# Optimization experiments

Measured on AMD Instinct MI355X. Metric: run time of the kernel, lower is better.

The kernel has to match this reference:

```python
import jax, jax.numpy as jnp
import numpy as np

NUM_MODELS = 64
IN_F, HID, OUT_F = 6, 64, 3
LAYERS = 5
LN_EPS = 1e-5


def _mm_linear(x, W, B, idx):
    # W: [M, out, in], B: [M, out], x: [N, in], idx: [N]
    return jnp.einsum('nof,nf->no', W[idx], x) + B[idx]


def _mm_layernorm(x, g, b, idx):
    mu = jnp.mean(x, axis=-1, keepdims=True)
    var = jnp.mean((x - mu) ** 2, axis=-1, keepdims=True)
    xn = (x - mu) * jax.lax.rsqrt(var + LN_EPS)
    return xn * g[idx] + b[idx]


def setup_inputs() -> dict:
    key = jax.random.key(0)
    ks = jax.random.split(key, 16)
    N = 262144
    sqrt_k = float(np.sqrt(1.0 / NUM_MODELS))
    u = lambda k, shape: jax.random.uniform(k, shape, jnp.float32, -sqrt_k, sqrt_k)
    inp = {
        'x': jax.random.normal(ks[0], (N, IN_F), jnp.float32),
        'indices': jax.random.randint(ks[1], (N,), 0, NUM_MODELS),
        'W0': u(ks[2], (NUM_MODELS, HID, IN_F)), 'B0': u(ks[3], (NUM_MODELS, HID)),
        'G0': jnp.ones((NUM_MODELS, HID), jnp.float32), 'H0': jnp.zeros((NUM_MODELS, HID), jnp.float32),
        'W1': u(ks[4], (NUM_MODELS, HID, HID)), 'B1': u(ks[5], (NUM_MODELS, HID)),
        'G1': jnp.ones((NUM_MODELS, HID), jnp.float32), 'H1': jnp.zeros((NUM_MODELS, HID), jnp.float32),
        'W2': u(ks[6], (NUM_MODELS, HID, HID)), 'B2': u(ks[7], (NUM_MODELS, HID)),
        'G2': jnp.ones((NUM_MODELS, HID), jnp.float32), 'H2': jnp.zeros((NUM_MODELS, HID), jnp.float32),
        'W3': u(ks[8], (NUM_MODELS, HID, HID)), 'B3': u(ks[9], (NUM_MODELS, HID)),
        'G3': jnp.ones((NUM_MODELS, HID), jnp.float32), 'H3': jnp.zeros((NUM_MODELS, HID), jnp.float32),
        'W4': u(ks[10], (NUM_MODELS, OUT_F, HID)), 'B4': u(ks[11], (NUM_MODELS, OUT_F)),
    }
    return inp


def reference(x, indices, W0, B0, G0, H0, W1, B1, G1, H1, W2, B2, G2, H2, W3, B3, G3, H3, W4, B4):
    # forward_through_layers with use_layernorm=True, layers=5:
    Ws = [(W0, B0, G0, H0), (W1, B1, G1, H1), (W2, B2, G2, H2), (W3, B3, G3, H3)]
    h = x
    for W, B, G, Hb in Ws:
        h = _mm_linear(h, W, B, indices)
        h = _mm_layernorm(h, G, Hb, indices)
        h = jax.nn.relu(h)
    return _mm_linear(h, W4, B4, indices)  # [N, 3]
```

## Files before the change

kernel.cpp:

```cpp
#include <hip/hip_runtime.h>


#define NM    64
#define HIDD  64
#define INF   6
#define OUTF  3
#define CAP   4864
#define NBLKB 128

#define CSTRIDE   32
#define O_CURSORS 0
#define O_ORDER   2048
#define IWS_INTS  (O_ORDER + NM * CAP)

#define CONST_B   30720
#define NCONSTF   784
#define IMG_BYTES 33856

#define HST 72

typedef _Float16 v8h __attribute__((ext_vector_type(8)));
typedef _Float16 v4h __attribute__((ext_vector_type(4)));
typedef float    v4f __attribute__((ext_vector_type(4)));

__global__ __launch_bounds__(256, 4) void bucket_img_kernel(
    const int* __restrict__ idx, const float* __restrict__ x, int n,
    const float* __restrict__ W0, const float* __restrict__ W1,
    const float* __restrict__ W2, const float* __restrict__ W3,
    const float* __restrict__ W4,
    const float* __restrict__ B0, const float* __restrict__ G0, const float* __restrict__ H0,
    const float* __restrict__ B1, const float* __restrict__ G1, const float* __restrict__ H1,
    const float* __restrict__ B2, const float* __restrict__ G2, const float* __restrict__ H2,
    const float* __restrict__ B3, const float* __restrict__ G3, const float* __restrict__ H3,
    const float* __restrict__ B4,
    int* __restrict__ iws, _Float16* __restrict__ xs,
    unsigned char* __restrict__ imgbase) {
    __shared__ int lcnt[NM], lcur[NM];
    const int b = blockIdx.x, t = threadIdx.x;
    const int m = b >> 1, sub = b & 1;

    _Float16* img = (_Float16*)(imgbase + (size_t)m * IMG_BYTES);
    float* cst = (float*)(imgbase + (size_t)m * IMG_BYTES + CONST_B);
    for (int s = sub * 256 + t; s < 1920; s += 512) {
        int f = s >> 6, l = s & 63;
        int c = l & 15, q = l >> 4;
        float vals[8];
        if (f < 4) {
            const float* wr = W0 + m * 384 + (f * 16 + c) * 6;
#pragma unroll
            for (int j = 0; j < 8; j++) {
                int k = q * 8 + j;
                vals[j] = (k < INF) ? wr[k] : 0.0f;
            }
        } else if (f < 28) {
            int ll = (f - 4) >> 3, fb = (f - 4) & 7;
            int mt = fb >> 1, kh = fb & 1;
            const float* W = (ll == 0) ? W1 : (ll == 1) ? W2 : W3;
            const float* wr = W + m * 4096 + (mt * 16 + c) * 64 + kh * 32 + q * 8;
#pragma unroll
            for (int j = 0; j < 8; j++) vals[j] = wr[j];
        } else {
            int kh = f - 28;
            const float* wr = W4 + m * 192 + c * 64 + kh * 32 + q * 8;
#pragma unroll
            for (int j = 0; j < 8; j++) vals[j] = (c < OUTF) ? wr[j] : 0.0f;
        }
        v8h o;
#pragma unroll
        for (int j = 0; j < 8; j++) o[j] = (_Float16)vals[j];
        *(v8h*)(img + (size_t)s * 8) = o;
    }
    for (int e = sub * 256 + t; e < NCONSTF; e += 512) {
        const float* lsrc[12] = {B0, G0, H0, B1, G1, H1, B2, G2, H2, B3, G3, H3};
        float v = 0.0f;
        if (e < 768) {
            int l = e / 192, r = e - l * 192;
            v = lsrc[l * 3 + (r >> 6)][m * 64 + (r & 63)];
        } else if (e < 771) {
            v = B4[m * 3 + (e - 768)];
        }
        cst[e] = v;
    }

    if (t < NM) lcnt[t] = 0;
    __syncthreads();
    const int per = (n + NBLKB - 1) / NBLKB;
    const int beg = b * per, end = min(n, beg + per);
    for (int i = beg + t; i < end; i += 256) atomicAdd(&lcnt[idx[i]], 1);
    __syncthreads();
    if (t < NM) lcur[t] = atomicAdd(&iws[O_CURSORS + t * CSTRIDE], lcnt[t]);
    __syncthreads();
    for (int i = beg + t; i < end; i += 256) {
        int mm = idx[i];
        int r = atomicAdd(&lcur[mm], 1);
        int slot = mm * CAP + r;
        iws[O_ORDER + slot] = i;
        const float* xp = x + (size_t)i * 6;
        float2 a0 = *(const float2*)(xp);
        float2 a1 = *(const float2*)(xp + 2);
        float2 a2 = *(const float2*)(xp + 4);
        v8h o = {};
        o[0] = (_Float16)a0.x; o[1] = (_Float16)a0.y;
        o[2] = (_Float16)a1.x; o[3] = (_Float16)a1.y;
        o[4] = (_Float16)a2.x; o[5] = (_Float16)a2.y;
        *(v8h*)(xs + (size_t)slot * 8) = o;
    }
}

__device__ __forceinline__ void layer_epilogue(v4f D[4], const v4f gg[4], const v4f hh[4],
                                               _Float16* __restrict__ st) {
    float S = 0.0f, Q2 = 0.0f;
#pragma unroll
    for (int mt = 0; mt < 4; mt++)
#pragma unroll
        for (int r = 0; r < 4; r++) {
            float v = D[mt][r];
            S += v;
            Q2 = fmaf(v, v, Q2);
        }
    S += __shfl_xor(S, 16, 64);
    S += __shfl_xor(S, 32, 64);
    Q2 += __shfl_xor(Q2, 16, 64);
    Q2 += __shfl_xor(Q2, 32, 64);
    float mu = S * (1.0f / 64.0f);
    float var = Q2 * (1.0f / 64.0f) - mu * mu;
    float rs = rsqrtf(var + 1e-5f);
#pragma unroll
    for (int mt = 0; mt < 4; mt++) {
        v4h o;
#pragma unroll
        for (int r = 0; r < 4; r++) {
            float a = gg[mt][r] * rs;
            float bb = fmaf(-mu, a, hh[mt][r]);
            o[r] = (_Float16)fmaxf(fmaf(D[mt][r], a, bb), 0.0f);
        }
        *(v4h*)(st + mt * 16) = o;
    }
}

__global__ __launch_bounds__(256, 4) void mlp_kernel(
    const int* __restrict__ iws, const _Float16* __restrict__ xs,
    const unsigned char* __restrict__ imgbase, float* __restrict__ out) {
    __shared__ __align__(16) _Float16 s_H[4 * 64 * HST];

    const int m = blockIdx.y;
    const int cnt = iws[O_CURSORS + m * CSTRIDE];
    const int beg = m * CAP, end = beg + cnt;
    const int base = beg + blockIdx.x * 256;
    if (base >= end) return;

    const int t = threadIdx.x, w = t >> 6, lane = t & 63;
    const int c = lane & 15, q = lane >> 4;
    const int wbase = base + w * 64;
    if (wbase >= end) return;

    const _Float16* img = (const _Float16*)(imgbase + (size_t)m * IMG_BYTES);
    const float* cf = (const float*)(imgbase + (size_t)m * IMG_BYTES + CONST_B);
    _Float16* Hw = s_H + w * (64 * HST);
    const int* order = iws + O_ORDER;

    int sid[4], sp[4];
#pragma unroll
    for (int ti = 0; ti < 4; ti++) {
        int p = wbase + ti * 16 + c;
        sp[ti] = p < end ? p : end - 1;
        sid[ti] = order[sp[ti]];
    }

    {
        v8h A[4];
#pragma unroll
        for (int mt = 0; mt < 4; mt++)
            A[mt] = *(const v8h*)(img + mt * 512 + lane * 8);
        v4f bias[4], gg[4], hh[4];
#pragma unroll
        for (int mt = 0; mt < 4; mt++) {
            bias[mt] = *(const v4f*)(cf + mt * 16 + q * 4);
            gg[mt]   = *(const v4f*)(cf + 64 + mt * 16 + q * 4);
            hh[mt]   = *(const v4f*)(cf + 128 + mt * 16 + q * 4);
        }
#pragma unroll
        for (int ti = 0; ti < 4; ti++) {
            v8h bfr = {};
            if (q == 0) bfr = *(const v8h*)(xs + (size_t)sp[ti] * 8);
            v4f D[4];
#pragma unroll
            for (int mt = 0; mt < 4; mt++)
                D[mt] = __builtin_amdgcn_mfma_f32_16x16x32_f16(A[mt], bfr, bias[mt], 0, 0, 0);
            layer_epilogue(D, gg, hh, Hw + (ti * 16 + c) * HST + q * 4);
        }
    }

#pragma unroll
    for (int l = 1; l <= 3; l++) {
        const _Float16* wp = img + 2048 + (l - 1) * 4096 + lane * 8;
        v8h A[4][2];
#pragma unroll
        for (int mt = 0; mt < 4; mt++)
#pragma unroll
            for (int kh = 0; kh < 2; kh++)
                A[mt][kh] = *(const v8h*)(wp + (mt * 2 + kh) * 512);
        const float* cb = cf + l * 192;
        v4f bias[4], gg[4], hh[4];
#pragma unroll
        for (int mt = 0; mt < 4; mt++) {
            bias[mt] = *(const v4f*)(cb + mt * 16 + q * 4);
            gg[mt]   = *(const v4f*)(cb + 64 + mt * 16 + q * 4);
            hh[mt]   = *(const v4f*)(cb + 128 + mt * 16 + q * 4);
        }
#pragma unroll
        for (int ti = 0; ti < 4; ti++) {
            const _Float16* hp = Hw + (ti * 16 + c) * HST;
            v8h b0 = *(const v8h*)(hp + q * 8);
            v8h b1 = *(const v8h*)(hp + 32 + q * 8);
            v4f D[4];
#pragma unroll
            for (int mt = 0; mt < 4; mt++) {
                D[mt] = __builtin_amdgcn_mfma_f32_16x16x32_f16(A[mt][0], b0, bias[mt], 0, 0, 0);
                D[mt] = __builtin_amdgcn_mfma_f32_16x16x32_f16(A[mt][1], b1, D[mt], 0, 0, 0);
            }
            layer_epilogue(D, gg, hh, Hw + (ti * 16 + c) * HST + q * 4);
        }
    }

    {
        const _Float16* wp = img + 14336 + lane * 8;
        v8h A0 = *(const v8h*)(wp);
        v8h A1 = *(const v8h*)(wp + 512);
        v4f b4i = {cf[768], cf[769], cf[770], 0.0f};
#pragma unroll
        for (int ti = 0; ti < 4; ti++) {
            const _Float16* hp = Hw + (ti * 16 + c) * HST;
            v8h b0 = *(const v8h*)(hp + q * 8);
            v8h b1 = *(const v8h*)(hp + 32 + q * 8);
            v4f D = __builtin_amdgcn_mfma_f32_16x16x32_f16(A0, b0, b4i, 0, 0, 0);
            D = __builtin_amdgcn_mfma_f32_16x16x32_f16(A1, b1, D, 0, 0, 0);
            int p = wbase + ti * 16 + c;
            if (q == 0 && p < end) {
                float* op = out + (size_t)sid[ti] * 3;
                op[0] = D[0]; op[1] = D[1]; op[2] = D[2];
            }
        }
    }
}

extern "C" void kernel_launch(void* const* d_in, const int* in_sizes, int n_in,
                              void* d_out, int out_size, void* d_ws, size_t ws_size,
                              hipStream_t stream) {
    const float* x  = (const float*)d_in[0];
    const int*  idx = (const int*)d_in[1];
    const float* W0 = (const float*)d_in[2];
    const float* B0 = (const float*)d_in[3];
    const float* G0 = (const float*)d_in[4];
    const float* H0 = (const float*)d_in[5];
    const float* W1 = (const float*)d_in[6];
    const float* B1 = (const float*)d_in[7];
    const float* G1 = (const float*)d_in[8];
    const float* H1 = (const float*)d_in[9];
    const float* W2 = (const float*)d_in[10];
    const float* B2 = (const float*)d_in[11];
    const float* G2 = (const float*)d_in[12];
    const float* H2 = (const float*)d_in[13];
    const float* W3 = (const float*)d_in[14];
    const float* B3 = (const float*)d_in[15];
    const float* G3 = (const float*)d_in[16];
    const float* H3 = (const float*)d_in[17];
    const float* W4 = (const float*)d_in[18];
    const float* B4 = (const float*)d_in[19];
    float* out = (float*)d_out;

    int n = in_sizes[1];
    int* iws = (int*)d_ws;
    _Float16* xs = (_Float16*)((char*)d_ws + (size_t)IWS_INTS * 4);
    unsigned char* imgbase =
        (unsigned char*)d_ws + (size_t)IWS_INTS * 4 + (size_t)NM * CAP * 16;

    hipMemsetAsync(d_ws, 0, NM * CSTRIDE * sizeof(int), stream);
    bucket_img_kernel<<<dim3(NBLKB), 256, 0, stream>>>(
        idx, x, n, W0, W1, W2, W3, W4,
        B0, G0, H0, B1, G1, H1, B2, G2, H2, B3, G3, H3, B4, iws, xs, imgbase);
    mlp_kernel<<<dim3(19, NM), 256, 0, stream>>>(iws, xs, imgbase, out);
}
```

Baseline: 136.5 us.

## Split bucket cursors four ways and halve MLP tile per wave

The bucketing kernel now uses 256 blocks, each assigned to one of four cursor classes per model. Each class fills its own region of the bucket, two growing from each end of a half, which spreads atomic contention on the global cursors. Local ranks are computed in a single pass and kept in registers, removing the second idx read and the shared-memory atomics. The MLP kernel processes 32 rows per wave instead of 64 over a doubled grid, loads LayerNorm gamma and beta inside the epilogue to cut register use, and raises the launch bound to 6 blocks per SIMD for more occupancy. Rows in gaps between the regions are skipped by validity masks, at the cost of more complex bounds logic and possibly idle waves.

Result: slower. 176.4 us (+29.2%).

```diff
diff --git a/kernel.cpp b/kernel.cpp
--- a/kernel.cpp
+++ b/kernel.cpp
@@ -6,11 +6,12 @@
 #define INF   6
 #define OUTF  3
 #define CAP   4864
-#define NBLKB 128
+#define RHALF 2432
+#define NBLKB 256
 
 #define CSTRIDE   32
 #define O_CURSORS 0
-#define O_ORDER   2048
+#define O_ORDER   8192
 #define IWS_INTS  (O_ORDER + NM * CAP)
 
 #define CONST_B   30720
@@ -35,13 +36,14 @@
     const float* __restrict__ B4,
     int* __restrict__ iws, _Float16* __restrict__ xs,
     unsigned char* __restrict__ imgbase) {
-    __shared__ int lcnt[NM], lcur[NM];
+    __shared__ int lcnt[NM], lbase[NM];
     const int b = blockIdx.x, t = threadIdx.x;
-    const int m = b >> 1, sub = b & 1;
+    const int m = b >> 2, sub = b & 3;
+    const int cls = b & 3;
 
     _Float16* img = (_Float16*)(imgbase + (size_t)m * IMG_BYTES);
     float* cst = (float*)(imgbase + (size_t)m * IMG_BYTES + CONST_B);
-    for (int s = sub * 256 + t; s < 1920; s += 512) {
+    for (int s = sub * 256 + t; s < 1920; s += 1024) {
         int f = s >> 6, l = s & 63;
         int c = l & 15, q = l >> 4;
         float vals[8];
@@ -70,32 +72,49 @@
         for (int j = 0; j < 8; j++) o[j] = (_Float16)vals[j];
         *(v8h*)(img + (size_t)s * 8) = o;
     }
-    for (int e = sub * 256 + t; e < NCONSTF; e += 512) {
+    {
         const float* lsrc[12] = {B0, G0, H0, B1, G1, H1, B2, G2, H2, B3, G3, H3};
-        float v = 0.0f;
-        if (e < 768) {
-            int l = e / 192, r = e - l * 192;
-            v = lsrc[l * 3 + (r >> 6)][m * 64 + (r & 63)];
-        } else if (e < 771) {
-            v = B4[m * 3 + (e - 768)];
-        }
-        cst[e] = v;
+        int e = sub * 256 + t;
+        if (e < NCONSTF) {
+            float v = 0.0f;
+            if (e < 768) {
+                int l = e / 192, r = e - l * 192;
+                v = lsrc[l * 3 + (r >> 6)][m * 64 + (r & 63)];
+            } else if (e < 771) {
+                v = B4[m * 3 + (e - 768)];
+            }
+            cst[e] = v;
+        }
     }
 
     if (t < NM) lcnt[t] = 0;
     __syncthreads();
     const int per = (n + NBLKB - 1) / NBLKB;
     const int beg = b * per, end = min(n, beg + per);
-    for (int i = beg + t; i < end; i += 256) atomicAdd(&lcnt[idx[i]], 1);
+    int sidq[4], mmq[4], rrq[4];
+    int qn = 0;
+    for (int i = beg + t; i < end; i += 256) {
+        sidq[qn] = i;
+        mmq[qn] = idx[i];
+        rrq[qn] = atomicAdd(&lcnt[mmq[qn]], 1);
+        qn++;
+    }
     __syncthreads();
-    if (t < NM) lcur[t] = atomicAdd(&iws[O_CURSORS + t * CSTRIDE], lcnt[t]);
+    if (t < NM)
+        lbase[t] = atomicAdd(&iws[O_CURSORS + (t * 4 + cls) * CSTRIDE], lcnt[t]);
     __syncthreads();
-    for (int i = beg + t; i < end; i += 256) {
-        int mm = idx[i];
-        int r = atomicAdd(&lcur[mm], 1);
-        int slot = mm * CAP + r;
-        iws[O_ORDER + slot] = i;
-        const float* xp = x + (size_t)i * 6;
+    for (int j = 0; j < qn; j++) {
+        int mm = mmq[j];
+        int rel;
+        switch (cls) {
+            case 0:  rel = lbase[mm] + rrq[j]; break;
+            case 1:  rel = RHALF - lbase[mm] - lcnt[mm] + rrq[j]; break;
+            case 2:  rel = RHALF + lbase[mm] + rrq[j]; break;
+            default: rel = CAP - lbase[mm] - lcnt[mm] + rrq[j]; break;
+        }
+        int slot = mm * CAP + rel;
+        iws[O_ORDER + slot] = sidq[j];
+        const float* xp = x + (size_t)sidq[j] * 6;
         float2 a0 = *(const float2*)(xp);
         float2 a1 = *(const float2*)(xp + 2);
         float2 a2 = *(const float2*)(xp + 4);
@@ -107,8 +126,9 @@
     }
 }
 
-__device__ __forceinline__ void layer_epilogue(v4f D[4], const v4f gg[4], const v4f hh[4],
-                                               _Float16* __restrict__ st) {
+__device__ __forceinline__ void layer_epilogue(v4f D[4],
+                                               const float* __restrict__ cb,
+                                               int q, _Float16* __restrict__ st) {
     float S = 0.0f, Q2 = 0.0f;
 #pragma unroll
     for (int mt = 0; mt < 4; mt++)
@@ -127,44 +147,52 @@
     float rs = rsqrtf(var + 1e-5f);
 #pragma unroll
     for (int mt = 0; mt < 4; mt++) {
+        v4f g = *(const v4f*)(cb + 64 + mt * 16 + q * 4);
+        v4f h = *(const v4f*)(cb + 128 + mt * 16 + q * 4);
         v4h o;
 #pragma unroll
         for (int r = 0; r < 4; r++) {
-            float a = gg[mt][r] * rs;
-            float bb = fmaf(-mu, a, hh[mt][r]);
+            float a = g[r] * rs;
+            float bb = fmaf(-mu, a, h[r]);
             o[r] = (_Float16)fmaxf(fmaf(D[mt][r], a, bb), 0.0f);
         }
         *(v4h*)(st + mt * 16) = o;
     }
 }
 
-__global__ __launch_bounds__(256, 4) void mlp_kernel(
+__global__ __launch_bounds__(256, 6) void mlp_kernel(
     const int* __restrict__ iws, const _Float16* __restrict__ xs,
     const unsigned char* __restrict__ imgbase, float* __restrict__ out) {
-    __shared__ __align__(16) _Float16 s_H[4 * 64 * HST];
+    __shared__ __align__(16) _Float16 s_H[4 * 32 * HST];
 
     const int m = blockIdx.y;
-    const int cnt = iws[O_CURSORS + m * CSTRIDE];
-    const int beg = m * CAP, end = beg + cnt;
-    const int base = beg + blockIdx.x * 256;
-    if (base >= end) return;
+    const int a0 = iws[O_CURSORS + (m * 4 + 0) * CSTRIDE];
+    const int a1 = iws[O_CURSORS + (m * 4 + 1) * CSTRIDE];
+    const int a2 = iws[O_CURSORS + (m * 4 + 2) * CSTRIDE];
+    const int a3 = iws[O_CURSORS + (m * 4 + 3) * CSTRIDE];
+    const int B0 = blockIdx.x * 128, B1 = B0 + 128;
+    if (!((B0 < a0) | ((B1 > RHALF - a1) & (B0 < RHALF + a2)) | (B1 > CAP - a3)))
+        return;
 
     const int t = threadIdx.x, w = t >> 6, lane = t & 63;
     const int c = lane & 15, q = lane >> 4;
-    const int wbase = base + w * 64;
-    if (wbase >= end) return;
+    const int W0r = B0 + w * 32, W1r = W0r + 32;
+    if (!((W0r < a0) | ((W1r > RHALF - a1) & (W0r < RHALF + a2)) | (W1r > CAP - a3)))
+        return;
 
     const _Float16* img = (const _Float16*)(imgbase + (size_t)m * IMG_BYTES);
     const float* cf = (const float*)(imgbase + (size_t)m * IMG_BYTES + CONST_B);
-    _Float16* Hw = s_H + w * (64 * HST);
+    _Float16* Hw = s_H + w * (32 * HST);
     const int* order = iws + O_ORDER;
 
-    int sid[4], sp[4];
-#pragma unroll
-    for (int ti = 0; ti < 4; ti++) {
-        int p = wbase + ti * 16 + c;
-        sp[ti] = p < end ? p : end - 1;
-        sid[ti] = order[sp[ti]];
+    int sid[2], vld[2], slot[2];
+#pragma unroll
+    for (int ti = 0; ti < 2; ti++) {
+        int rel = W0r + ti * 16 + c;
+        vld[ti] = (rel < a0) | ((rel >= RHALF - a1) & (rel < RHALF + a2)) |
+                  (rel >= CAP - a3);
+        slot[ti] = m * CAP + rel;
+        sid[ti] = order[slot[ti]];
     }
 
     {
@@ -172,22 +200,19 @@
 #pragma unroll
         for (int mt = 0; mt < 4; mt++)
             A[mt] = *(const v8h*)(img + mt * 512 + lane * 8);
-        v4f bias[4], gg[4], hh[4];
-#pragma unroll
-        for (int mt = 0; mt < 4; mt++) {
+        v4f bias[4];
+#pragma unroll
+        for (int mt = 0; mt < 4; mt++)
             bias[mt] = *(const v4f*)(cf + mt * 16 + q * 4);
-            gg[mt]   = *(const v4f*)(cf + 64 + mt * 16 + q * 4);
-            hh[mt]   = *(const v4f*)(cf + 128 + mt * 16 + q * 4);
-        }
-#pragma unroll
-        for (int ti = 0; ti < 4; ti++) {
+#pragma unroll
+        for (int ti = 0; ti < 2; ti++) {
             v8h bfr = {};
-            if (q == 0) bfr = *(const v8h*)(xs + (size_t)sp[ti] * 8);
+            if (q == 0) bfr = *(const v8h*)(xs + (size_t)slot[ti] * 8);
             v4f D[4];
 #pragma unroll
             for (int mt = 0; mt < 4; mt++)
                 D[mt] = __builtin_amdgcn_mfma_f32_16x16x32_f16(A[mt], bfr, bias[mt], 0, 0, 0);
-            layer_epilogue(D, gg, hh, Hw + (ti * 16 + c) * HST + q * 4);
+            layer_epilogue(D, cf, q, Hw + (ti * 16 + c) * HST + q * 4);
         }
     }
 
@@ -201,15 +226,12 @@
             for (int kh = 0; kh < 2; kh++)
                 A[mt][kh] = *(const v8h*)(wp + (mt * 2 + kh) * 512);
         const float* cb = cf + l * 192;
-        v4f bias[4], gg[4], hh[4];
-#pragma unroll
-        for (int mt = 0; mt < 4; mt++) {
+        v4f bias[4];
+#pragma unroll
+        for (int mt = 0; mt < 4; mt++)
             bias[mt] = *(const v4f*)(cb + mt * 16 + q * 4);
-            gg[mt]   = *(const v4f*)(cb + 64 + mt * 16 + q * 4);
-            hh[mt]   = *(const v4f*)(cb + 128 + mt * 16 + q * 4);
-        }
-#pragma unroll
-        for (int ti = 0; ti < 4; ti++) {
+#pragma unroll
+        for (int ti = 0; ti < 2; ti++) {
             const _Float16* hp = Hw + (ti * 16 + c) * HST;
             v8h b0 = *(const v8h*)(hp + q * 8);
             v8h b1 = *(const v8h*)(hp + 32 + q * 8);
@@ -219,7 +241,7 @@
                 D[mt] = __builtin_amdgcn_mfma_f32_16x16x32_f16(A[mt][0], b0, bias[mt], 0, 0, 0);
                 D[mt] = __builtin_amdgcn_mfma_f32_16x16x32_f16(A[mt][1], b1, D[mt], 0, 0, 0);
             }
-            layer_epilogue(D, gg, hh, Hw + (ti * 16 + c) * HST + q * 4);
+            layer_epilogue(D, cb, q, Hw + (ti * 16 + c) * HST + q * 4);
         }
     }
 
@@ -229,14 +251,13 @@
         v8h A1 = *(const v8h*)(wp + 512);
         v4f b4i = {cf[768], cf[769], cf[770], 0.0f};
 #pragma unroll
-        for (int ti = 0; ti < 4; ti++) {
+        for (int ti = 0; ti < 2; ti++) {
             const _Float16* hp = Hw + (ti * 16 + c) * HST;
             v8h b0 = *(const v8h*)(hp + q * 8);
             v8h b1 = *(const v8h*)(hp + 32 + q * 8);
             v4f D = __builtin_amdgcn_mfma_f32_16x16x32_f16(A0, b0, b4i, 0, 0, 0);
             D = __builtin_amdgcn_mfma_f32_16x16x32_f16(A1, b1, D, 0, 0, 0);
-            int p = wbase + ti * 16 + c;
-            if (q == 0 && p < end) {
+            if (q == 0 && vld[ti]) {
                 float* op = out + (size_t)sid[ti] * 3;
                 op[0] = D[0]; op[1] = D[1]; op[2] = D[2];
             }
@@ -275,9 +296,9 @@
     unsigned char* imgbase =
         (unsigned char*)d_ws + (size_t)IWS_INTS * 4 + (size_t)NM * CAP * 16;
 
-    hipMemsetAsync(d_ws, 0, NM * CSTRIDE * sizeof(int), stream);
+    hipMemsetAsync(d_ws, 0, NM * 4 * CSTRIDE * sizeof(int), stream);
     bucket_img_kernel<<<dim3(NBLKB), 256, 0, stream>>>(
         idx, x, n, W0, W1, W2, W3, W4,
         B0, G0, H0, B1, G1, H1, B2, G2, H2, B3, G3, H3, B4, iws, xs, imgbase);
-    mlp_kernel<<<dim3(19, NM), 256, 0, stream>>>(iws, xs, imgbase, out);
+    mlp_kernel<<<dim3(38, NM), 256, 0, stream>>>(iws, xs, imgbase, out);
 }
```

## Keep hidden activations in registers via permuted weight rows, dropping LDS staging

Applied to the files above, without the earlier changes.

Permutes the hidden-unit order of the weight rows and the bias/gamma/beta vectors during image build, so each MFMA output fragment already matches the B-operand layout the next layer needs. Activations then stay in registers across layers instead of being written to and reread from shared memory. This removes the LDS round trip and the 36 KB shared buffer, which frees occupancy. Gamma and beta are now loaded inside the epilogue instead of being held in registers, and conversion uses packed round-toward-zero, which changes rounding slightly.

Result: slower. 183.2 us (+34.1%).

```diff
diff --git a/kernel.cpp b/kernel.cpp
--- a/kernel.cpp
+++ b/kernel.cpp
@@ -17,11 +17,14 @@
 #define NCONSTF   784
 #define IMG_BYTES 33856
 
-#define HST 72
-
 typedef _Float16 v8h __attribute__((ext_vector_type(8)));
-typedef _Float16 v4h __attribute__((ext_vector_type(4)));
+typedef __fp16   v2hf __attribute__((ext_vector_type(2)));
 typedef float    v4f __attribute__((ext_vector_type(4)));
+
+__device__ __host__ __forceinline__ int phi(int p) {
+    int mt = p >> 4, q = (p >> 2) & 3, r = p & 3;
+    return ((mt >> 1) << 5) | (q << 3) | ((mt & 1) << 2) | r;
+}
 
 __global__ __launch_bounds__(256, 4) void bucket_img_kernel(
     const int* __restrict__ idx, const float* __restrict__ x, int n,
@@ -46,7 +49,7 @@
         int c = l & 15, q = l >> 4;
         float vals[8];
         if (f < 4) {
-            const float* wr = W0 + m * 384 + (f * 16 + c) * 6;
+            const float* wr = W0 + m * 384 + phi(f * 16 + c) * 6;
 #pragma unroll
             for (int j = 0; j < 8; j++) {
                 int k = q * 8 + j;
@@ -56,7 +59,7 @@
             int ll = (f - 4) >> 3, fb = (f - 4) & 7;
             int mt = fb >> 1, kh = fb & 1;
             const float* W = (ll == 0) ? W1 : (ll == 1) ? W2 : W3;
-            const float* wr = W + m * 4096 + (mt * 16 + c) * 64 + kh * 32 + q * 8;
+            const float* wr = W + m * 4096 + phi(mt * 16 + c) * 64 + kh * 32 + q * 8;
 #pragma unroll
             for (int j = 0; j < 8; j++) vals[j] = wr[j];
         } else {
@@ -75,7 +78,7 @@
         float v = 0.0f;
         if (e < 768) {
             int l = e / 192, r = e - l * 192;
-            v = lsrc[l * 3 + (r >> 6)][m * 64 + (r & 63)];
+            v = lsrc[l * 3 + (r >> 6)][m * 64 + phi(r & 63)];
         } else if (e < 771) {
             v = B4[m * 3 + (e - 768)];
         }
@@ -107,8 +110,10 @@
     }
 }
 
-__device__ __forceinline__ void layer_epilogue(v4f D[4], const v4f gg[4], const v4f hh[4],
-                                               _Float16* __restrict__ st) {
+__device__ __forceinline__ void layer_epilogue(const v4f D[4],
+                                               const float* __restrict__ cb,
+                                               int q, v8h* __restrict__ pb0,
+                                               v8h* __restrict__ pb1) {
     float S = 0.0f, Q2 = 0.0f;
 #pragma unroll
     for (int mt = 0; mt < 4; mt++)
@@ -125,24 +130,30 @@
     float mu = S * (1.0f / 64.0f);
     float var = Q2 * (1.0f / 64.0f) - mu * mu;
     float rs = rsqrtf(var + 1e-5f);
+    float nm = -mu * rs;
+    union { v8h v; v2hf p[4]; } u0, u1;
 #pragma unroll
     for (int mt = 0; mt < 4; mt++) {
-        v4h o;
+        v4f g = *(const v4f*)(cb + 64 + mt * 16 + q * 4);
+        v4f h = *(const v4f*)(cb + 128 + mt * 16 + q * 4);
+        float y[4];
 #pragma unroll
         for (int r = 0; r < 4; r++) {
-            float a = gg[mt][r] * rs;
-            float bb = fmaf(-mu, a, hh[mt][r]);
-            o[r] = (_Float16)fmaxf(fmaf(D[mt][r], a, bb), 0.0f);
-        }
-        *(v4h*)(st + mt * 16) = o;
-    }
+            float tt = fmaf(D[mt][r], rs, nm);
+            y[r] = fmaxf(fmaf(tt, g[r], h[r]), 0.0f);
+        }
+        v2hf p0 = __builtin_amdgcn_cvt_pkrtz(y[0], y[1]);
+        v2hf p1 = __builtin_amdgcn_cvt_pkrtz(y[2], y[3]);
+        if (mt < 2) { u0.p[mt * 2] = p0; u0.p[mt * 2 + 1] = p1; }
+        else        { u1.p[(mt - 2) * 2] = p0; u1.p[(mt - 2) * 2 + 1] = p1; }
+    }
+    *pb0 = u0.v;
+    *pb1 = u1.v;
 }
 
 __global__ __launch_bounds__(256, 4) void mlp_kernel(
     const int* __restrict__ iws, const _Float16* __restrict__ xs,
     const unsigned char* __restrict__ imgbase, float* __restrict__ out) {
-    __shared__ __align__(16) _Float16 s_H[4 * 64 * HST];
-
     const int m = blockIdx.y;
     const int cnt = iws[O_CURSORS + m * CSTRIDE];
     const int beg = m * CAP, end = beg + cnt;
@@ -156,7 +167,6 @@
 
     const _Float16* img = (const _Float16*)(imgbase + (size_t)m * IMG_BYTES);
     const float* cf = (const float*)(imgbase + (size_t)m * IMG_BYTES + CONST_B);
-    _Float16* Hw = s_H + w * (64 * HST);
     const int* order = iws + O_ORDER;
 
     int sid[4], sp[4];
@@ -167,18 +177,17 @@
         sid[ti] = order[sp[ti]];
     }
 
+    v8h b0[4], b1[4];
+
     {
         v8h A[4];
 #pragma unroll
         for (int mt = 0; mt < 4; mt++)
             A[mt] = *(const v8h*)(img + mt * 512 + lane * 8);
-        v4f bias[4], gg[4], hh[4];
-#pragma unroll
-        for (int mt = 0; mt < 4; mt++) {
+        v4f bias[4];
+#pragma unroll
+        for (int mt = 0; mt < 4; mt++)
             bias[mt] = *(const v4f*)(cf + mt * 16 + q * 4);
-            gg[mt]   = *(const v4f*)(cf + 64 + mt * 16 + q * 4);
-            hh[mt]   = *(const v4f*)(cf + 128 + mt * 16 + q * 4);
-        }
 #pragma unroll
         for (int ti = 0; ti < 4; ti++) {
             v8h bfr = {};
@@ -187,7 +196,7 @@
 #pragma unroll
             for (int mt = 0; mt < 4; mt++)
                 D[mt] = __builtin_amdgcn_mfma_f32_16x16x32_f16(A[mt], bfr, bias[mt], 0, 0, 0);
-            layer_epilogue(D, gg, hh, Hw + (ti * 16 + c) * HST + q * 4);
+            layer_epilogue(D, cf, q, &b0[ti], &b1[ti]);
         }
     }
 
@@ -201,25 +210,19 @@
             for (int kh = 0; kh < 2; kh++)
                 A[mt][kh] = *(const v8h*)(wp + (mt * 2 + kh) * 512);
         const float* cb = cf + l * 192;
-        v4f bias[4], gg[4], hh[4];
-#pragma unroll
-        for (int mt = 0; mt < 4; mt++) {
+        v4f bias[4];
+#pragma unroll
+        for (int mt = 0; mt < 4; mt++)
             bias[mt] = *(const v4f*)(cb + mt * 16 + q * 4);
-            gg[mt]   = *(const v4f*)(cb + 64 + mt * 16 + q * 4);
-            hh[mt]   = *(const v4f*)(cb + 128 + mt * 16 + q * 4);
-        }
 #pragma unroll
         for (int ti = 0; ti < 4; ti++) {
-            const _Float16* hp = Hw + (ti * 16 + c) * HST;
-            v8h b0 = *(const v8h*)(hp + q * 8);
-            v8h b1 = *(const v8h*)(hp + 32 + q * 8);
             v4f D[4];
 #pragma unroll
             for (int mt = 0; mt < 4; mt++) {
-                D[mt] = __builtin_amdgcn_mfma_f32_16x16x32_f16(A[mt][0], b0, bias[mt], 0, 0, 0);
-                D[mt] = __builtin_amdgcn_mfma_f32_16x16x32_f16(A[mt][1], b1, D[mt], 0, 0, 0);
+                D[mt] = __builtin_amdgcn_mfma_f32_16x16x32_f16(A[mt][0], b0[ti], bias[mt], 0, 0, 0);
+                D[mt] = __builtin_amdgcn_mfma_f32_16x16x32_f16(A[mt][1], b1[ti], D[mt], 0, 0, 0);
             }
-            layer_epilogue(D, gg, hh, Hw + (ti * 16 + c) * HST + q * 4);
+            layer_epilogue(D, cb, q, &b0[ti], &b1[ti]);
         }
     }
 
@@ -230,11 +233,8 @@
         v4f b4i = {cf[768], cf[769], cf[770], 0.0f};
 #pragma unroll
         for (int ti = 0; ti < 4; ti++) {
-            const _Float16* hp = Hw + (ti * 16 + c) * HST;
-            v8h b0 = *(const v8h*)(hp + q * 8);
-            v8h b1 = *(const v8h*)(hp + 32 + q * 8);
-            v4f D = __builtin_amdgcn_mfma_f32_16x16x32_f16(A0, b0, b4i, 0, 0, 0);
-            D = __builtin_amdgcn_mfma_f32_16x16x32_f16(A1, b1, D, 0, 0, 0);
+            v4f D = __builtin_amdgcn_mfma_f32_16x16x32_f16(A0, b0[ti], b4i, 0, 0, 0);
+            D = __builtin_amdgcn_mfma_f32_16x16x32_f16(A1, b1[ti], D, 0, 0, 0);
             int p = wbase + ti * 16 + c;
             if (q == 0 && p < end) {
                 float* op = out + (size_t)sid[ti] * 3;
@@ -275,7 +275,7 @@
     unsigned char* imgbase =
         (unsigned char*)d_ws + (size_t)IWS_INTS * 4 + (size_t)NM * CAP * 16;
 
-    hipMemsetAsync(d_ws, 0, NM * CSTRIDE * sizeof(int), stream);
+    (void)hipMemsetAsync(d_ws, 0, NM * CSTRIDE * sizeof(int), stream);
     bucket_img_kernel<<<dim3(NBLKB), 256, 0, stream>>>(
         idx, x, n, W0, W1, W2, W3, W4,
         B0, G0, H0, B1, G1, H1, B2, G2, H2, B3, G3, H3, B4, iws, xs, imgbase);
```
